# Kernel optimization log

Hardware: AMD Instinct MI355X
Metric: run time of the kernel (lower is better)

## Reference

```python
import jax, jax.numpy as jnp
import numpy as np

N = 524288
H = 128
EPS = 1e-4
SYMP_N = 32  # min(N, 32)
# loss weights from init_kwargs
W_RECON, W_CONS, W_EVO, W_SYMP, W_GAUGE = 1.0, 10.0, 5.0, 0.1, 5.0


def _mlp(x, W1, b1, W2, b2, W3, b3):
    h = jnp.tanh(x @ W1 + b1)
    h = jnp.tanh(h @ W2 + b2)
    return h @ W3 + b3


def _encode(p, q, params):
    out = _mlp(jnp.stack([p, q], axis=-1), *params)  # [N,2]
    return out[:, 0], out[:, 1]


def _decode(P, Q, params):
    out = _mlp(jnp.stack([P, Q], axis=-1), *params)
    return out[:, 0], out[:, 1]


def setup_inputs() -> dict:
    key = jax.random.key(0)
    ks = jax.random.split(key, 24)
    f32 = jnp.float32

    def nrm(k, shape, scale=1.0):
        return (scale * jax.random.normal(k, shape, dtype=f32))

    inp = {
        'p0': nrm(ks[0], (N,)),
        'q0': nrm(ks[1], (N,)),
        'p1': nrm(ks[2], (N,)),
        'q1': nrm(ks[3], (N,)),
        'omega_values': jax.random.uniform(ks[4], (N,), dtype=f32, minval=0.5, maxval=2.0),
        'dt': jnp.asarray(0.05, dtype=f32),
        'P_true': nrm(ks[5], (N,)),
        'Q_true': nrm(ks[6], (N,)),
        # encoder params (2 -> H -> H -> 2), fan-in scaled init
        'enc_W1': nrm(ks[7], (2, H), 1.0 / np.sqrt(2.0)),
        'enc_b1': jnp.zeros((H,), f32),
        'enc_W2': nrm(ks[8], (H, H), 1.0 / np.sqrt(H)),
        'enc_b2': jnp.zeros((H,), f32),
        'enc_W3': nrm(ks[9], (H, 2), 1.0 / np.sqrt(H)),
        'enc_b3': jnp.zeros((2,), f32),
        # decoder params
        'dec_W1': nrm(ks[10], (2, H), 1.0 / np.sqrt(2.0)),
        'dec_b1': jnp.zeros((H,), f32),
        'dec_W2': nrm(ks[11], (H, H), 1.0 / np.sqrt(H)),
        'dec_b2': jnp.zeros((H,), f32),
        'dec_W3': nrm(ks[12], (H, 2), 1.0 / np.sqrt(H)),
        'dec_b3': jnp.zeros((2,), f32),
    }
    return inp


def _loss(p0, q0, p1, q1, omega_values, dt, P_true, Q_true, enc, dec):
    P0, Q0 = _encode(p0, q0, enc)
    P1, Q1 = _encode(p1, q1, enc)
    p0_recon, q0_recon = _decode(P0, Q0, dec)

    recon_loss = jnp.mean((p0 - p0_recon) ** 2 + (q0 - q0_recon) ** 2)
    conservation_loss = jnp.mean((P0 - P1) ** 2)
    evolution_loss = jnp.mean(1.0 - jnp.cos((Q1 - Q0) - omega_values * dt))

    # symplectic loss: batched central finite differences over first 32 samples
    pi, qi = p0[:SYMP_N], q0[:SYMP_N]
    pp = jnp.concatenate([pi + EPS, pi - EPS, pi, pi])          # [4*32]
    qq = jnp.concatenate([qi, qi, qi + EPS, qi - EPS])
    P, Q = _encode(pp, qq, enc)
    P_pp, P_pm, P_qp, P_qm = jnp.split(P, 4)
    Q_pp, Q_pm, Q_qp, Q_qm = jnp.split(Q, 4)
    inv2e = 1.0 / (2.0 * EPS)
    dP_dp = (P_pp - P_pm) * inv2e
    dP_dq = (P_qp - P_qm) * inv2e
    dQ_dp = (Q_pp - Q_pm) * inv2e
    dQ_dq = (Q_qp - Q_qm) * inv2e
    pb = dP_dq * dQ_dp - dP_dp * dQ_dq
    symplectic_loss = jnp.mean((jnp.abs(pb) - 1.0) ** 2)

    gauge_loss = jnp.mean((P0 - P_true) ** 2) + jnp.mean(1.0 - jnp.cos(Q0 - Q_true))

    total = (W_RECON * recon_loss + W_CONS * conservation_loss
             + W_EVO * evolution_loss + W_SYMP * symplectic_loss
             + W_GAUGE * gauge_loss)
    return jnp.stack([total, recon_loss, conservation_loss,
                      evolution_loss, symplectic_loss, gauge_loss])


def reference(p0, q0, p1, q1, omega_values, dt, P_true, Q_true,
              enc_W1, enc_b1, enc_W2, enc_b2, enc_W3, enc_b3,
              dec_W1, dec_b1, dec_W2, dec_b2, dec_W3, dec_b3):
    enc = (enc_W1, enc_b1, enc_W2, enc_b2, enc_W3, enc_b3)
    dec = (dec_W1, dec_b1, dec_W2, dec_b2, dec_W3, dec_b3)
    return _loss(p0, q0, p1, q1, omega_values, dt, P_true, Q_true, enc, dec)
```

## Files before the change

kernel.cpp:

```cpp
#include <hip/hip_runtime.h>
#include <stdint.h>
#include <math.h>


constexpr float EPS_FD = 1e-4f;
constexpr float K2LOG2E = 2.8853900817779268f;
constexpr int NBLK = 256;

typedef float f32x4 __attribute__((ext_vector_type(4)));
typedef short s16x8 __attribute__((ext_vector_type(8)));

__device__ __forceinline__ float tanh_pre(float x) {
  float e = __builtin_amdgcn_exp2f(x);
  return 1.0f - 2.0f * __builtin_amdgcn_rcpf(e + 1.0f);
}
__device__ __forceinline__ float cos_fast(float x) {
  return __builtin_amdgcn_cosf(x * 0.15915494309189535f);
}
__device__ __forceinline__ unsigned bf16rne(float f) {
  union { float f; unsigned u; } v; v.f = f;
  return (v.u + 0x7FFFu + ((v.u >> 16) & 1u)) >> 16;
}
__device__ __forceinline__ unsigned pack2rne(float a, float b) {
  return bf16rne(a) | (bf16rne(b) << 16);
}
__device__ __forceinline__ unsigned packbf(float lo, float hi) {
  union { float f; unsigned u; } a, b; a.f = lo; b.f = hi;
  return __builtin_amdgcn_perm(b.u + 0x8000u, a.u + 0x8000u, 0x07060302u);
}

template<bool SCAT>
__device__ __forceinline__ void layer1_frags(
    float pe, float qe, unsigned* hrow,
    float w100, float w101, float w110, float w111, float b10, float b11,
    int lane, int quad, int l15, s16x8 (&A)[4])
{
#pragma unroll
  for (int ee = 0; ee < 16; ee++) {
    int src = SCAT ? (16 * (ee >> 2) + (ee & 3)) : ee;
    float p = __shfl(pe, src, 64);
    float q = __shfl(qe, src, 64);
    float a0 = tanh_pre(fmaf(p, w100, fmaf(q, w110, b10)));
    float a1 = tanh_pre(fmaf(p, w101, fmaf(q, w111, b11)));
    hrow[ee * 68 + lane] = packbf(a0, a1);
  }
  __builtin_amdgcn_wave_barrier();
#pragma unroll
  for (int s = 0; s < 4; s++) {
    uint4 u = *reinterpret_cast<const uint4*>(&hrow[l15 * 68 + 16 * s + 4 * quad]);
    A[s] = *reinterpret_cast<s16x8*>(&u);
  }
  __builtin_amdgcn_wave_barrier();
}

__device__ __forceinline__ void enc_pair(
    float p0e, float q0e, float p1e, float q1e,
    unsigned* hrow, const uint4* Bf, const float* epi,
    float w100, float w101, float w110, float w111, float b10, float b11,
    int lane, int quad, int l15,
    float& P0v, float& Q0v, float& P1v, float& Q1v)
{
  s16x8 A0[4], A1[4];
  layer1_frags<false>(p0e, q0e, hrow, w100, w101, w110, w111, b10, b11,
                      lane, quad, l15, A0);
  layer1_frags<false>(p1e, q1e, hrow, w100, w101, w110, w111, b10, b11,
                      lane, quad, l15, A1);

  float sP0[4] = {0,0,0,0}, sQ0[4] = {0,0,0,0};
  float sP1[4] = {0,0,0,0}, sQ1[4] = {0,0,0,0};
#pragma unroll
  for (int t = 0; t < 8; t++) {
    float b2v = epi[16 * t + l15];
    f32x4 acc0 = {b2v, b2v, b2v, b2v};
    f32x4 acc1 = {b2v, b2v, b2v, b2v};
#pragma unroll
    for (int s = 0; s < 4; s++) {
      uint4 bu = Bf[(s * 8 + t) * 64 + lane];
      s16x8 Bv = *reinterpret_cast<s16x8*>(&bu);
      acc0 = __builtin_amdgcn_mfma_f32_16x16x32_bf16(A0[s], Bv, acc0, 0, 0, 0);
      acc1 = __builtin_amdgcn_mfma_f32_16x16x32_bf16(A1[s], Bv, acc1, 0, 0, 0);
    }
    float w3Pv = epi[128 + 16 * t + l15];
    float w3Qv = epi[256 + 16 * t + l15];
#pragma unroll
    for (int r = 0; r < 4; r++) {
      float h0 = tanh_pre(acc0[r]);
      float h1 = tanh_pre(acc1[r]);
      sP0[r] = fmaf(h0, w3Pv, sP0[r]); sQ0[r] = fmaf(h0, w3Qv, sQ0[r]);
      sP1[r] = fmaf(h1, w3Pv, sP1[r]); sQ1[r] = fmaf(h1, w3Qv, sQ1[r]);
    }
  }
#pragma unroll
  for (int m = 1; m < 16; m <<= 1) {
#pragma unroll
    for (int r = 0; r < 4; r++) {
      sP0[r] += __shfl_xor(sP0[r], m, 64);
      sQ0[r] += __shfl_xor(sQ0[r], m, 64);
      sP1[r] += __shfl_xor(sP1[r], m, 64);
      sQ1[r] += __shfl_xor(sQ1[r], m, 64);
    }
  }
  P0v = (l15 == 0) ? sP0[0] : (l15 == 1) ? sP0[1] : (l15 == 2) ? sP0[2] : sP0[3];
  Q0v = (l15 == 0) ? sQ0[0] : (l15 == 1) ? sQ0[1] : (l15 == 2) ? sQ0[2] : sQ0[3];
  P1v = (l15 == 0) ? sP1[0] : (l15 == 1) ? sP1[1] : (l15 == 2) ? sP1[2] : sP1[3];
  Q1v = (l15 == 0) ? sQ1[0] : (l15 == 1) ? sQ1[1] : (l15 == 2) ? sQ1[2] : sQ1[3];
}

__device__ __forceinline__ void dec_pass(
    float pe, float qe, unsigned* hrow, const uint4* Bf, const float* epi,
    float w100, float w101, float w110, float w111, float b10, float b11,
    int lane, int quad, int l15, float& vP, float& vQ)
{
  s16x8 A[4];
  layer1_frags<true>(pe, qe, hrow, w100, w101, w110, w111, b10, b11,
                     lane, quad, l15, A);
  float sP[4] = {0,0,0,0}, sQ[4] = {0,0,0,0};
#pragma unroll
  for (int t = 0; t < 8; t++) {
    float b2v = epi[16 * t + l15];
    f32x4 acc = {b2v, b2v, b2v, b2v};
#pragma unroll
    for (int s = 0; s < 4; s++) {
      uint4 bu = Bf[(s * 8 + t) * 64 + lane];
      s16x8 Bv = *reinterpret_cast<s16x8*>(&bu);
      acc = __builtin_amdgcn_mfma_f32_16x16x32_bf16(A[s], Bv, acc, 0, 0, 0);
    }
    float w3Pv = epi[128 + 16 * t + l15];
    float w3Qv = epi[256 + 16 * t + l15];
#pragma unroll
    for (int r = 0; r < 4; r++) {
      float h = tanh_pre(acc[r]);
      sP[r] = fmaf(h, w3Pv, sP[r]);
      sQ[r] = fmaf(h, w3Qv, sQ[r]);
    }
  }
#pragma unroll
  for (int m = 1; m < 16; m <<= 1) {
#pragma unroll
    for (int r = 0; r < 4; r++) {
      sP[r] += __shfl_xor(sP[r], m, 64);
      sQ[r] += __shfl_xor(sQ[r], m, 64);
    }
  }
  vP = (l15 == 0) ? sP[0] : (l15 == 1) ? sP[1] : (l15 == 2) ? sP[2] : sP[3];
  vQ = (l15 == 0) ? sQ[0] : (l15 == 1) ? sQ[1] : (l15 == 2) ? sQ[2] : sQ[3];
}

__global__ __launch_bounds__(1024, 1) void mlp_main(
    const float* __restrict__ p0, const float* __restrict__ q0,
    const float* __restrict__ p1, const float* __restrict__ q1,
    const float* __restrict__ eW1, const float* __restrict__ eb1,
    const float* __restrict__ eW2, const float* __restrict__ eb2,
    const float* __restrict__ eW3, const float* __restrict__ eb3,
    const float* __restrict__ dW1, const float* __restrict__ db1,
    const float* __restrict__ dW2, const float* __restrict__ db2,
    const float* __restrict__ dW3, const float* __restrict__ db3,
    const float* __restrict__ omega, const float* __restrict__ Pt,
    const float* __restrict__ Qt, const float* __restrict__ dtp,
    float* __restrict__ acc5, unsigned* __restrict__ counter,
    float* __restrict__ PQ, float* __restrict__ out, int n)
{
  __shared__ uint4 BfE[2048];
  __shared__ uint4 BfD[2048];
  __shared__ unsigned h1s[16][16 * 68 + 4];
  __shared__ float encEpi[384];
  __shared__ float decEpi[384];
  __shared__ float red[16][5];
  __shared__ unsigned lastflag;

  int tid = threadIdx.x;
#pragma unroll
  for (int it = 0; it < 8; it++) {
    int id = tid + it * 1024;
    int jj = id & 3, ln = (id >> 2) & 63, f = id >> 8;
    int s = f >> 3, t = f & 7;
    int k   = 32 * s + 8 * (ln >> 4) + 2 * jj;
    int col = 16 * t + (ln & 15);
    ((unsigned*)BfE)[id] = pack2rne(eW2[k * 128 + col] * K2LOG2E,
                                    eW2[(k + 1) * 128 + col] * K2LOG2E);
    ((unsigned*)BfD)[id] = pack2rne(dW2[k * 128 + col] * K2LOG2E,
                                    dW2[(k + 1) * 128 + col] * K2LOG2E);
  }
  if (tid < 128) {
    encEpi[tid]       = eb2[tid] * K2LOG2E;
    encEpi[128 + tid] = eW3[2 * tid];
    encEpi[256 + tid] = eW3[2 * tid + 1];
  } else if (tid < 256) {
    int u = tid - 128;
    decEpi[u]       = db2[u] * K2LOG2E;
    decEpi[128 + u] = dW3[2 * u];
    decEpi[256 + u] = dW3[2 * u + 1];
  }

  int wave = tid >> 6, lane = tid & 63;
  int quad = lane >> 4, l15 = lane & 15;

  float ew100 = eW1[2 * lane] * K2LOG2E,       ew101 = eW1[2 * lane + 1] * K2LOG2E;
  float ew110 = eW1[128 + 2 * lane] * K2LOG2E, ew111 = eW1[128 + 2 * lane + 1] * K2LOG2E;
  float eb10 = eb1[2 * lane] * K2LOG2E, eb11 = eb1[2 * lane + 1] * K2LOG2E;
  float dw100 = dW1[2 * lane] * K2LOG2E,       dw101 = dW1[2 * lane + 1] * K2LOG2E;
  float dw110 = dW1[128 + 2 * lane] * K2LOG2E, dw111 = dW1[128 + 2 * lane + 1] * K2LOG2E;
  float db10 = db1[2 * lane] * K2LOG2E, db11 = db1[2 * lane + 1] * K2LOG2E;
  float eb3P = eb3[0], eb3Q = eb3[1];
  float db3P = db3[0], db3Q = db3[1];
  float dt = dtp[0];
  float s0 = 0.f, s1 = 0.f, s2 = 0.f, s3 = 0.f, s4 = 0.f;
  __syncthreads();

  int nwaves = gridDim.x * 16;
  int gwave  = blockIdx.x * 16 + wave;
  int ntiles = (n + 15) >> 4;
  unsigned* hrow = &h1s[wave][0];

  if (gwave < 128) {
    int r = gwave;
    int m = r & 31, c = r >> 5;
    float p = p0[m], q = q0[m];
    p += (c == 0) ? EPS_FD : (c == 1) ? -EPS_FD : 0.f;
    q += (c == 2) ? EPS_FD : (c == 3) ? -EPS_FD : 0.f;
    float* hf = (float*)hrow;
    int t0 = 2 * lane, t1 = 2 * lane + 1;
    float h0 = tanhf(fmaf(p, eW1[t0], fmaf(q, eW1[128 + t0], eb1[t0])));
    float h1v = tanhf(fmaf(p, eW1[t1], fmaf(q, eW1[128 + t1], eb1[t1])));
    hf[t0] = h0; hf[t1] = h1v;
    __builtin_amdgcn_wave_barrier();
    float a0 = eb2[t0], a1 = eb2[t1];
#pragma unroll 8
    for (int k = 0; k < 128; k++) {
      float hk = hf[k];
      a0 = fmaf(hk, eW2[k * 128 + t0], a0);
      a1 = fmaf(hk, eW2[k * 128 + t1], a1);
    }
    float g0 = tanhf(a0), g1 = tanhf(a1);
    float cP = fmaf(g0, eW3[2 * t0],     g1 * eW3[2 * t1]);
    float cQ = fmaf(g0, eW3[2 * t0 + 1], g1 * eW3[2 * t1 + 1]);
#pragma unroll
    for (int mm = 1; mm < 64; mm <<= 1) {
      cP += __shfl_xor(cP, mm, 64);
      cQ += __shfl_xor(cQ, mm, 64);
    }
    if (lane == 0) {
      atomicExch(&PQ[2 * r],     cP + eb3P);
      atomicExch(&PQ[2 * r + 1], cQ + eb3Q);
    }
    __builtin_amdgcn_wave_barrier();
  }

  for (int tile = gwave; tile < ntiles; tile += nwaves) {
    int base = tile * 16;
    int e = base + l15; if (e >= n) e = n - 1;
    float p0e = p0[e], q0e = q0[e];
    float p1e = p1[e], q1e = q1[e];
    int o = base + quad * 4 + l15;
    int o16 = base + quad * 4 + (l15 & 3);
    if (o16 >= n) o16 = n - 1;
    float Lom = omega[o16], LPt = Pt[o16], LQt = Qt[o16];
    float Lp0 = p0[o16],    Lq0 = q0[o16];

    float P0v, Q0v, P1v, Q1v, RPv, RQv;
    enc_pair(p0e, q0e, p1e, q1e, hrow, BfE, encEpi,
             ew100, ew101, ew110, ew111, eb10, eb11,
             lane, quad, l15, P0v, Q0v, P1v, Q1v);
    P0v += eb3P; Q0v += eb3Q;
    P1v += eb3P; Q1v += eb3Q;
    dec_pass(P0v, Q0v, hrow, BfD, decEpi,
             dw100, dw101, dw110, dw111, db10, db11,
             lane, quad, l15, RPv, RQv);
    RPv += db3P; RQv += db3Q;

    if (l15 < 4 && o < n) {
      float dp = Lp0 - RPv, dq = Lq0 - RQv;
      s0 += dp * dp + dq * dq;
      float d1 = P0v - P1v; s1 += d1 * d1;
      s2 += 1.0f - cos_fast(Q1v - Q0v - Lom * dt);
      float g = P0v - LPt; s3 += g * g;
      s4 += 1.0f - cos_fast(Q0v - LQt);
    }
  }

#pragma unroll
  for (int m = 1; m < 64; m <<= 1) {
    s0 += __shfl_xor(s0, m, 64);
    s1 += __shfl_xor(s1, m, 64);
    s2 += __shfl_xor(s2, m, 64);
    s3 += __shfl_xor(s3, m, 64);
    s4 += __shfl_xor(s4, m, 64);
  }
  if (lane == 0) {
    red[wave][0] = s0; red[wave][1] = s1; red[wave][2] = s2;
    red[wave][3] = s3; red[wave][4] = s4;
  }
  __syncthreads();
  if (tid == 0) {
#pragma unroll
    for (int i = 0; i < 5; i++) {
      float v = 0.f;
#pragma unroll
      for (int w = 0; w < 16; w++) v += red[w][i];
      atomicAdd(&acc5[i], v);
    }
    __threadfence();
    unsigned prev = atomicAdd(counter, 1u);
    lastflag = (prev == gridDim.x - 1) ? 1u : 0u;
  }
  __syncthreads();
  if (lastflag) {
    __threadfence();
    if (tid < 64) {
      float v = 0.f;
      if (tid < 32) {
        float Ppp = atomicAdd(&PQ[2 * tid], 0.f);
        float Qpp = atomicAdd(&PQ[2 * tid + 1], 0.f);
        float Ppm = atomicAdd(&PQ[2 * (32 + tid)], 0.f);
        float Qpm = atomicAdd(&PQ[2 * (32 + tid) + 1], 0.f);
        float Pqp = atomicAdd(&PQ[2 * (64 + tid)], 0.f);
        float Qqp = atomicAdd(&PQ[2 * (64 + tid) + 1], 0.f);
        float Pqm = atomicAdd(&PQ[2 * (96 + tid)], 0.f);
        float Qqm = atomicAdd(&PQ[2 * (96 + tid) + 1], 0.f);
        float inv2e = 1.0f / (2.0f * EPS_FD);
        float dPdp = (Ppp - Ppm) * inv2e, dPdq = (Pqp - Pqm) * inv2e;
        float dQdp = (Qpp - Qpm) * inv2e, dQdq = (Qqp - Qqm) * inv2e;
        float pb = dPdq * dQdp - dPdp * dQdq;
        float d = fabsf(pb) - 1.0f;
        v = d * d;
      }
#pragma unroll
      for (int m = 1; m < 64; m <<= 1) v += __shfl_xor(v, m, 64);
      if (tid == 0) {
        float inv_n = 1.0f / (float)n;
        float recon = atomicAdd(&acc5[0], 0.f) * inv_n;
        float cons  = atomicAdd(&acc5[1], 0.f) * inv_n;
        float evo   = atomicAdd(&acc5[2], 0.f) * inv_n;
        float gauge = (atomicAdd(&acc5[3], 0.f) + atomicAdd(&acc5[4], 0.f)) * inv_n;
        float symp  = v * (1.0f / 32.0f);
        float total = recon + 10.0f * cons + 5.0f * evo + 0.1f * symp + 5.0f * gauge;
        out[0] = total; out[1] = recon; out[2] = cons;
        out[3] = evo;   out[4] = symp;  out[5] = gauge;
      }
    }
  }
}

extern "C" void kernel_launch(void* const* d_in, const int* in_sizes, int n_in,
                              void* d_out, int out_size, void* d_ws, size_t ws_size,
                              hipStream_t stream)
{
  const float* p0    = (const float*)d_in[0];
  const float* q0    = (const float*)d_in[1];
  const float* p1    = (const float*)d_in[2];
  const float* q1    = (const float*)d_in[3];
  const float* omega = (const float*)d_in[4];
  const float* dtp   = (const float*)d_in[5];
  const float* Pt    = (const float*)d_in[6];
  const float* Qt    = (const float*)d_in[7];
  const float* encW1 = (const float*)d_in[8];
  const float* encb1 = (const float*)d_in[9];
  const float* encW2 = (const float*)d_in[10];
  const float* encb2 = (const float*)d_in[11];
  const float* encW3 = (const float*)d_in[12];
  const float* encb3 = (const float*)d_in[13];
  const float* decW1 = (const float*)d_in[14];
  const float* decb1 = (const float*)d_in[15];
  const float* decW2 = (const float*)d_in[16];
  const float* decb2 = (const float*)d_in[17];
  const float* decW3 = (const float*)d_in[18];
  const float* decb3 = (const float*)d_in[19];

  int n = in_sizes[0];
  float* acc5 = (float*)d_ws;
  unsigned* counter = (unsigned*)(acc5 + 8);
  float* PQ = (float*)(acc5 + 16);

  hipMemsetAsync(acc5, 0, 64, stream);

  mlp_main<<<NBLK, 1024, 0, stream>>>(
      p0, q0, p1, q1,
      encW1, encb1, encW2, encb2, encW3, encb3,
      decW1, decb1, decW2, decb2, decW3, decb3,
      omega, Pt, Qt, dtp, acc5, counter, PQ, (float*)d_out, n);
}
```

Before: 266.4 us.

## Prepack W2 fragments in a prep kernel and read from global to raise occupancy

Adds a small prep kernel that converts the encoder and decoder W2 into bf16 MFMA fragments in workspace and zeroes the accumulators, replacing the memset. The main kernel then reads B fragments from global/L2 instead of holding 64KB in LDS, which allows more resident blocks; the launch uses 512 blocks with launch bounds allowing 8. The MFMA operands are swapped so each lane holds one output column, which removes the 16-lane shuffle reductions and per-row selects and uses a 2-step quad reduction instead. The risk is higher global/L2 traffic for the weight fragments in the inner loop, and the path depends on workspace size.

```diff
diff --git a/kernel.cpp b/kernel.cpp
--- a/kernel.cpp
+++ b/kernel.cpp
@@ -5,7 +5,6 @@
 
 constexpr float EPS_FD = 1e-4f;
 constexpr float K2LOG2E = 2.8853900817779268f;
-constexpr int NBLK = 256;
 
 typedef float f32x4 __attribute__((ext_vector_type(4)));
 typedef short s16x8 __attribute__((ext_vector_type(8)));
@@ -28,8 +27,12 @@
   union { float f; unsigned u; } a, b; a.f = lo; b.f = hi;
   return __builtin_amdgcn_perm(b.u + 0x8000u, a.u + 0x8000u, 0x07060302u);
 }
-
-template<bool SCAT>
+__device__ __forceinline__ float qred(float v) {
+  v += __shfl_xor(v, 16, 64);
+  v += __shfl_xor(v, 32, 64);
+  return v;
+}
+
 __device__ __forceinline__ void layer1_frags(
     float pe, float qe, unsigned* hrow,
     float w100, float w101, float w110, float w111, float b10, float b11,
@@ -37,9 +40,8 @@
 {
 #pragma unroll
   for (int ee = 0; ee < 16; ee++) {
-    int src = SCAT ? (16 * (ee >> 2) + (ee & 3)) : ee;
-    float p = __shfl(pe, src, 64);
-    float q = __shfl(qe, src, 64);
+    float p = __shfl(pe, ee, 64);
+    float q = __shfl(qe, ee, 64);
     float a0 = tanh_pre(fmaf(p, w100, fmaf(q, w110, b10)));
     float a1 = tanh_pre(fmaf(p, w101, fmaf(q, w111, b11)));
     hrow[ee * 68 + lane] = packbf(a0, a1);
@@ -55,98 +57,98 @@
 
 __device__ __forceinline__ void enc_pair(
     float p0e, float q0e, float p1e, float q1e,
-    unsigned* hrow, const uint4* Bf, const float* epi,
+    unsigned* hrow, const uint4* __restrict__ Bf, const float* epi,
     float w100, float w101, float w110, float w111, float b10, float b11,
     int lane, int quad, int l15,
     float& P0v, float& Q0v, float& P1v, float& Q1v)
 {
   s16x8 A0[4], A1[4];
-  layer1_frags<false>(p0e, q0e, hrow, w100, w101, w110, w111, b10, b11,
-                      lane, quad, l15, A0);
-  layer1_frags<false>(p1e, q1e, hrow, w100, w101, w110, w111, b10, b11,
-                      lane, quad, l15, A1);
-
-  float sP0[4] = {0,0,0,0}, sQ0[4] = {0,0,0,0};
-  float sP1[4] = {0,0,0,0}, sQ1[4] = {0,0,0,0};
+  layer1_frags(p0e, q0e, hrow, w100, w101, w110, w111, b10, b11,
+               lane, quad, l15, A0);
+  layer1_frags(p1e, q1e, hrow, w100, w101, w110, w111, b10, b11,
+               lane, quad, l15, A1);
+
+  float sP0 = 0.f, sQ0 = 0.f, sP1 = 0.f, sQ1 = 0.f;
 #pragma unroll
   for (int t = 0; t < 8; t++) {
-    float b2v = epi[16 * t + l15];
-    f32x4 acc0 = {b2v, b2v, b2v, b2v};
-    f32x4 acc1 = {b2v, b2v, b2v, b2v};
+    f32x4 acc0 = *reinterpret_cast<const f32x4*>(&epi[16 * t + 4 * quad]);
+    f32x4 acc1 = acc0;
 #pragma unroll
     for (int s = 0; s < 4; s++) {
       uint4 bu = Bf[(s * 8 + t) * 64 + lane];
       s16x8 Bv = *reinterpret_cast<s16x8*>(&bu);
-      acc0 = __builtin_amdgcn_mfma_f32_16x16x32_bf16(A0[s], Bv, acc0, 0, 0, 0);
-      acc1 = __builtin_amdgcn_mfma_f32_16x16x32_bf16(A1[s], Bv, acc1, 0, 0, 0);
-    }
-    float w3Pv = epi[128 + 16 * t + l15];
-    float w3Qv = epi[256 + 16 * t + l15];
+      acc0 = __builtin_amdgcn_mfma_f32_16x16x32_bf16(Bv, A0[s], acc0, 0, 0, 0);
+      acc1 = __builtin_amdgcn_mfma_f32_16x16x32_bf16(Bv, A1[s], acc1, 0, 0, 0);
+    }
+    f32x4 w3a = *reinterpret_cast<const f32x4*>(&epi[128 + 32 * t + 8 * quad]);
+    f32x4 w3b = *reinterpret_cast<const f32x4*>(&epi[128 + 32 * t + 8 * quad + 4]);
 #pragma unroll
     for (int r = 0; r < 4; r++) {
+      float wP = (r == 0) ? w3a[0] : (r == 1) ? w3a[2] : (r == 2) ? w3b[0] : w3b[2];
+      float wQ = (r == 0) ? w3a[1] : (r == 1) ? w3a[3] : (r == 2) ? w3b[1] : w3b[3];
       float h0 = tanh_pre(acc0[r]);
       float h1 = tanh_pre(acc1[r]);
-      sP0[r] = fmaf(h0, w3Pv, sP0[r]); sQ0[r] = fmaf(h0, w3Qv, sQ0[r]);
-      sP1[r] = fmaf(h1, w3Pv, sP1[r]); sQ1[r] = fmaf(h1, w3Qv, sQ1[r]);
-    }
-  }
-#pragma unroll
-  for (int m = 1; m < 16; m <<= 1) {
-#pragma unroll
-    for (int r = 0; r < 4; r++) {
-      sP0[r] += __shfl_xor(sP0[r], m, 64);
-      sQ0[r] += __shfl_xor(sQ0[r], m, 64);
-      sP1[r] += __shfl_xor(sP1[r], m, 64);
-      sQ1[r] += __shfl_xor(sQ1[r], m, 64);
-    }
-  }
-  P0v = (l15 == 0) ? sP0[0] : (l15 == 1) ? sP0[1] : (l15 == 2) ? sP0[2] : sP0[3];
-  Q0v = (l15 == 0) ? sQ0[0] : (l15 == 1) ? sQ0[1] : (l15 == 2) ? sQ0[2] : sQ0[3];
-  P1v = (l15 == 0) ? sP1[0] : (l15 == 1) ? sP1[1] : (l15 == 2) ? sP1[2] : sP1[3];
-  Q1v = (l15 == 0) ? sQ1[0] : (l15 == 1) ? sQ1[1] : (l15 == 2) ? sQ1[2] : sQ1[3];
+      sP0 = fmaf(h0, wP, sP0); sQ0 = fmaf(h0, wQ, sQ0);
+      sP1 = fmaf(h1, wP, sP1); sQ1 = fmaf(h1, wQ, sQ1);
+    }
+  }
+  P0v = qred(sP0); Q0v = qred(sQ0);
+  P1v = qred(sP1); Q1v = qred(sQ1);
 }
 
 __device__ __forceinline__ void dec_pass(
-    float pe, float qe, unsigned* hrow, const uint4* Bf, const float* epi,
+    float pe, float qe, unsigned* hrow, const uint4* __restrict__ Bf,
+    const float* epi,
     float w100, float w101, float w110, float w111, float b10, float b11,
     int lane, int quad, int l15, float& vP, float& vQ)
 {
   s16x8 A[4];
-  layer1_frags<true>(pe, qe, hrow, w100, w101, w110, w111, b10, b11,
-                     lane, quad, l15, A);
-  float sP[4] = {0,0,0,0}, sQ[4] = {0,0,0,0};
+  layer1_frags(pe, qe, hrow, w100, w101, w110, w111, b10, b11,
+               lane, quad, l15, A);
+  float sP = 0.f, sQ = 0.f;
 #pragma unroll
   for (int t = 0; t < 8; t++) {
-    float b2v = epi[16 * t + l15];
-    f32x4 acc = {b2v, b2v, b2v, b2v};
+    f32x4 acc = *reinterpret_cast<const f32x4*>(&epi[16 * t + 4 * quad]);
 #pragma unroll
     for (int s = 0; s < 4; s++) {
       uint4 bu = Bf[(s * 8 + t) * 64 + lane];
       s16x8 Bv = *reinterpret_cast<s16x8*>(&bu);
-      acc = __builtin_amdgcn_mfma_f32_16x16x32_bf16(A[s], Bv, acc, 0, 0, 0);
-    }
-    float w3Pv = epi[128 + 16 * t + l15];
-    float w3Qv = epi[256 + 16 * t + l15];
+      acc = __builtin_amdgcn_mfma_f32_16x16x32_bf16(Bv, A[s], acc, 0, 0, 0);
+    }
+    f32x4 w3a = *reinterpret_cast<const f32x4*>(&epi[128 + 32 * t + 8 * quad]);
+    f32x4 w3b = *reinterpret_cast<const f32x4*>(&epi[128 + 32 * t + 8 * quad + 4]);
 #pragma unroll
     for (int r = 0; r < 4; r++) {
+      float wP = (r == 0) ? w3a[0] : (r == 1) ? w3a[2] : (r == 2) ? w3b[0] : w3b[2];
+      float wQ = (r == 0) ? w3a[1] : (r == 1) ? w3a[3] : (r == 2) ? w3b[1] : w3b[3];
       float h = tanh_pre(acc[r]);
-      sP[r] = fmaf(h, w3Pv, sP[r]);
-      sQ[r] = fmaf(h, w3Qv, sQ[r]);
-    }
-  }
-#pragma unroll
-  for (int m = 1; m < 16; m <<= 1) {
-#pragma unroll
-    for (int r = 0; r < 4; r++) {
-      sP[r] += __shfl_xor(sP[r], m, 64);
-      sQ[r] += __shfl_xor(sQ[r], m, 64);
-    }
-  }
-  vP = (l15 == 0) ? sP[0] : (l15 == 1) ? sP[1] : (l15 == 2) ? sP[2] : sP[3];
-  vQ = (l15 == 0) ? sQ[0] : (l15 == 1) ? sQ[1] : (l15 == 2) ? sQ[2] : sQ[3];
-}
-
-__global__ __launch_bounds__(1024, 1) void mlp_main(
+      sP = fmaf(h, wP, sP);
+      sQ = fmaf(h, wQ, sQ);
+    }
+  }
+  vP = qred(sP); vQ = qred(sQ);
+}
+
+__global__ __launch_bounds__(1024) void prep_frags(
+    const float* __restrict__ eW2, const float* __restrict__ dW2,
+    unsigned* __restrict__ BfE, unsigned* __restrict__ BfD,
+    float* __restrict__ acc5)
+{
+  int id = blockIdx.x * 1024 + threadIdx.x;
+  if (blockIdx.x == 0 && threadIdx.x < 16)
+    ((unsigned*)acc5)[threadIdx.x] = 0u;
+  int jj = id & 3, ln = (id >> 2) & 63, f = id >> 8;
+  int s = f >> 3, t = f & 7;
+  int k   = 32 * s + 8 * (ln >> 4) + 2 * jj;
+  int col = 16 * t + (ln & 15);
+  BfE[id] = pack2rne(eW2[k * 128 + col] * K2LOG2E,
+                     eW2[(k + 1) * 128 + col] * K2LOG2E);
+  BfD[id] = pack2rne(dW2[k * 128 + col] * K2LOG2E,
+                     dW2[(k + 1) * 128 + col] * K2LOG2E);
+}
+
+template<bool GB>
+__global__ __launch_bounds__(1024, GB ? 8 : 1) void mlp_main(
     const float* __restrict__ p0, const float* __restrict__ q0,
     const float* __restrict__ p1, const float* __restrict__ q1,
     const float* __restrict__ eW1, const float* __restrict__ eb1,
@@ -157,11 +159,11 @@
     const float* __restrict__ dW3, const float* __restrict__ db3,
     const float* __restrict__ omega, const float* __restrict__ Pt,
     const float* __restrict__ Qt, const float* __restrict__ dtp,
+    const uint4* __restrict__ BfEg, const uint4* __restrict__ BfDg,
     float* __restrict__ acc5, unsigned* __restrict__ counter,
     float* __restrict__ PQ, float* __restrict__ out, int n)
 {
-  __shared__ uint4 BfE[2048];
-  __shared__ uint4 BfD[2048];
+  __shared__ uint4 BfL[GB ? 2 : 4096];
   __shared__ unsigned h1s[16][16 * 68 + 4];
   __shared__ float encEpi[384];
   __shared__ float decEpi[384];
@@ -169,28 +171,31 @@
   __shared__ unsigned lastflag;
 
   int tid = threadIdx.x;
-#pragma unroll
-  for (int it = 0; it < 8; it++) {
-    int id = tid + it * 1024;
-    int jj = id & 3, ln = (id >> 2) & 63, f = id >> 8;
-    int s = f >> 3, t = f & 7;
-    int k   = 32 * s + 8 * (ln >> 4) + 2 * jj;
-    int col = 16 * t + (ln & 15);
-    ((unsigned*)BfE)[id] = pack2rne(eW2[k * 128 + col] * K2LOG2E,
-                                    eW2[(k + 1) * 128 + col] * K2LOG2E);
-    ((unsigned*)BfD)[id] = pack2rne(dW2[k * 128 + col] * K2LOG2E,
-                                    dW2[(k + 1) * 128 + col] * K2LOG2E);
-  }
-  if (tid < 128) {
-    encEpi[tid]       = eb2[tid] * K2LOG2E;
-    encEpi[128 + tid] = eW3[2 * tid];
-    encEpi[256 + tid] = eW3[2 * tid + 1];
-  } else if (tid < 256) {
-    int u = tid - 128;
-    decEpi[u]       = db2[u] * K2LOG2E;
-    decEpi[128 + u] = dW3[2 * u];
-    decEpi[256 + u] = dW3[2 * u + 1];
-  }
+  if constexpr (!GB) {
+    unsigned* BE = (unsigned*)&BfL[0];
+    unsigned* BD = (unsigned*)&BfL[2048];
+#pragma unroll
+    for (int it = 0; it < 8; it++) {
+      int id = tid + it * 1024;
+      int jj = id & 3, ln = (id >> 2) & 63, f = id >> 8;
+      int s = f >> 3, t = f & 7;
+      int k   = 32 * s + 8 * (ln >> 4) + 2 * jj;
+      int col = 16 * t + (ln & 15);
+      BE[id] = pack2rne(eW2[k * 128 + col] * K2LOG2E,
+                        eW2[(k + 1) * 128 + col] * K2LOG2E);
+      BD[id] = pack2rne(dW2[k * 128 + col] * K2LOG2E,
+                        dW2[(k + 1) * 128 + col] * K2LOG2E);
+    }
+  }
+  if (tid < 128)      encEpi[tid] = eb2[tid] * K2LOG2E;
+  else if (tid < 256) decEpi[tid - 128] = db2[tid - 128] * K2LOG2E;
+  else if (tid < 512) encEpi[128 + tid - 256] = eW3[tid - 256];
+  else if (tid < 768) decEpi[128 + tid - 512] = dW3[tid - 512];
+
+  const uint4* BfE;
+  const uint4* BfD;
+  if constexpr (GB) { BfE = BfEg; BfD = BfDg; }
+  else              { BfE = &BfL[0]; BfD = &BfL[2048]; }
 
   int wave = tid >> 6, lane = tid & 63;
   int quad = lane >> 4, l15 = lane & 15;
@@ -251,11 +256,7 @@
     int e = base + l15; if (e >= n) e = n - 1;
     float p0e = p0[e], q0e = q0[e];
     float p1e = p1[e], q1e = q1[e];
-    int o = base + quad * 4 + l15;
-    int o16 = base + quad * 4 + (l15 & 3);
-    if (o16 >= n) o16 = n - 1;
-    float Lom = omega[o16], LPt = Pt[o16], LQt = Qt[o16];
-    float Lp0 = p0[o16],    Lq0 = q0[o16];
+    float Lom = omega[e], LPt = Pt[e], LQt = Qt[e];
 
     float P0v, Q0v, P1v, Q1v, RPv, RQv;
     enc_pair(p0e, q0e, p1e, q1e, hrow, BfE, encEpi,
@@ -268,8 +269,8 @@
              lane, quad, l15, RPv, RQv);
     RPv += db3P; RQv += db3Q;
 
-    if (l15 < 4 && o < n) {
-      float dp = Lp0 - RPv, dq = Lq0 - RQv;
+    if (quad == 0 && base + l15 < n) {
+      float dp = p0e - RPv, dq = q0e - RQv;
       s0 += dp * dp + dq * dq;
       float d1 = P0v - P1v; s1 += d1 * d1;
       s2 += 1.0f - cos_fast(Q1v - Q0v - Lom * dt);
@@ -370,12 +371,28 @@
   float* acc5 = (float*)d_ws;
   unsigned* counter = (unsigned*)(acc5 + 8);
   float* PQ = (float*)(acc5 + 16);
-
-  hipMemsetAsync(acc5, 0, 64, stream);
-
-  mlp_main<<<NBLK, 1024, 0, stream>>>(
-      p0, q0, p1, q1,
-      encW1, encb1, encW2, encb2, encW3, encb3,
-      decW1, decb1, decW2, decb2, decW3, decb3,
-      omega, Pt, Qt, dtp, acc5, counter, PQ, (float*)d_out, n);
-}
+  unsigned* BfEg = (unsigned*)((char*)d_ws + 4096);
+  unsigned* BfDg = BfEg + 8192;
+
+  bool gb = ws_size >= (size_t)(4096 + 2 * 32768);
+
+  if (gb) {
+    prep_frags<<<8, 1024, 0, stream>>>(encW2, decW2, BfEg, BfDg, acc5);
+    mlp_main<true><<<512, 1024, 0, stream>>>(
+        p0, q0, p1, q1,
+        encW1, encb1, encW2, encb2, encW3, encb3,
+        decW1, decb1, decW2, decb2, decW3, decb3,
+        omega, Pt, Qt, dtp,
+        (const uint4*)BfEg, (const uint4*)BfDg,
+        acc5, counter, PQ, (float*)d_out, n);
+  } else {
+    hipMemsetAsync(acc5, 0, 64, stream);
+    mlp_main<false><<<256, 1024, 0, stream>>>(
+        p0, q0, p1, q1,
+        encW1, encb1, encW2, encb2, encW3, encb3,
+        decW1, decb1, decW2, decb2, decW3, decb3,
+        omega, Pt, Qt, dtp,
+        nullptr, nullptr,
+        acc5, counter, PQ, (float*)d_out, n);
+  }
+}
```

Result: slower. 1.057 ms (+296.6%).
